# Kernel optimization log

Hardware: AMD Instinct MI355X
Metric: run time of the kernel (lower is better)

## Reference

```python
import jax, jax.numpy as jnp
import numpy as np

B, S, D, H = 8, 1024, 512, 8  # batch, max_mol_real, d_model, num_heads
DH = D // 2                   # per-branch width
DEPTH = D // H                # per-head depth (64)
HH = H // 2                   # heads per branch (4)


def setup_inputs() -> dict:
    key = jax.random.key(0)
    ks = jax.random.split(key, 16)
    sc = 0.02
    inp = {
        'x': jax.random.normal(ks[0], (B, S, D), jnp.float32),
        'mask': jnp.zeros((B, 1, 1, S), jnp.float32),
        'adj': jax.random.uniform(ks[1], (B, S, S), jnp.float32),
        'dist': jax.random.uniform(ks[2], (B, S, S), jnp.float32),
        # dist branch projections (Dense(d_model/2))
        'Wq_dist': jax.random.normal(ks[3], (D, DH), jnp.float32) * sc,
        'bq_dist': jnp.zeros((DH,), jnp.float32),
        'Wk_dist': jax.random.normal(ks[4], (D, DH), jnp.float32) * sc,
        'bk_dist': jnp.zeros((DH,), jnp.float32),
        'Wv_dist': jax.random.normal(ks[5], (D, DH), jnp.float32) * sc,
        'bv_dist': jnp.zeros((DH,), jnp.float32),
        # adj branch projections
        'Wq_adj': jax.random.normal(ks[6], (D, DH), jnp.float32) * sc,
        'bq_adj': jnp.zeros((DH,), jnp.float32),
        'Wk_adj': jax.random.normal(ks[7], (D, DH), jnp.float32) * sc,
        'bk_adj': jnp.zeros((DH,), jnp.float32),
        'Wv_adj': jax.random.normal(ks[8], (D, DH), jnp.float32) * sc,
        'bv_adj': jnp.zeros((DH,), jnp.float32),
        # output projection Dense(d_model)
        'Wo': jax.random.normal(ks[9], (D, D), jnp.float32) * sc,
        'bo': jnp.zeros((D,), jnp.float32),
    }
    return inp


def _split_heads(t):
    # (B, S, HH*DEPTH) -> (B, HH, S, DEPTH)
    return t.reshape(B, S, HH, DEPTH).transpose(0, 2, 1, 3)


def _sdpa_ad(q, k, v, mask, adj=None, dist=None):
    # mask: (B,1,1,S) -> additive -1e9 * mask, per original code
    m = mask * -1000000000.0
    logits = jnp.einsum('bhqd,bhkd->bhqk', q, k) / jnp.sqrt(jnp.float32(DEPTH))
    w = jax.nn.softmax(logits + m, axis=-1)  # (B, HH, S, S)
    if adj is not None:
        w = w * adj[:, None, :, :]
    if dist is not None:  # dist_value == 'original'
        w = w * jax.nn.softmax(dist[:, None, :, :] + m, axis=-1)
    return jnp.einsum('bhqk,bhkd->bhqd', w, v)


def reference(x, mask, adj, dist,
              Wq_dist, bq_dist, Wk_dist, bk_dist, Wv_dist, bv_dist,
              Wq_adj, bq_adj, Wk_adj, bk_adj, Wv_adj, bv_adj,
              Wo, bo):
    # ----- dist branch -----
    qd = _split_heads(x @ Wq_dist + bq_dist)
    kd = _split_heads(x @ Wk_dist + bk_dist)
    vd = _split_heads(x @ Wv_dist + bv_dist)
    od = _sdpa_ad(qd, kd, vd, mask, adj=None, dist=dist)
    od = od.transpose(0, 2, 1, 3).reshape(B, S, DH)
    # ----- adj branch -----
    qa = _split_heads(x @ Wq_adj + bq_adj)
    ka = _split_heads(x @ Wk_adj + bk_adj)
    va = _split_heads(x @ Wv_adj + bv_adj)
    oa = _sdpa_ad(qa, ka, va, mask, adj=adj, dist=None)
    oa = oa.transpose(0, 2, 1, 3).reshape(B, S, DH)
    # ----- concat + output dense -----
    cat = jnp.concatenate([od, oa], axis=-1)  # (B, S, D)
    return cat @ Wo + bo
```

## Files before the change

### kernel.cpp

```cpp
#include <hip/hip_runtime.h>

typedef __attribute__((ext_vector_type(8))) short bf16x8;
typedef __attribute__((ext_vector_type(4))) float f32x4;
typedef unsigned short ushortT;

#define B_   8
#define S_   1024
#define D_   512
#define DH_  256
#define NH_  4
#define DEP_ 64
#define LOG2E 1.4426950408889634f

__device__ __forceinline__ unsigned short f2bf(float f){
    unsigned u = __builtin_bit_cast(unsigned, f);
    u += 0x7fffu + ((u>>16)&1u);
    return (unsigned short)(u>>16);
}
__device__ __forceinline__ float bf2f(ushortT v){
    unsigned u = ((unsigned)v)<<16;
    return __builtin_bit_cast(float, u);
}
__device__ __forceinline__ int swz(int row,int cb){ return (row<<7) + (cb ^ ((row&7)<<4)); }

__global__ __launch_bounds__(256) void prep_x(const float* __restrict__ x, ushortT* __restrict__ xb){
    size_t t = (size_t)blockIdx.x*256 + threadIdx.x;
    float4 v = *(const float4*)(x + t*4);
    ushort4 o; o.x=f2bf(v.x); o.y=f2bf(v.y); o.z=f2bf(v.z); o.w=f2bf(v.w);
    *(ushort4*)(xb + t*4) = o;
}

__global__ __launch_bounds__(256) void prep_w(
    const float* __restrict__ W0, const float* __restrict__ W1, const float* __restrict__ W2,
    const float* __restrict__ W3, const float* __restrict__ W4, const float* __restrict__ W5,
    const float* __restrict__ B0, const float* __restrict__ B1, const float* __restrict__ B2,
    const float* __restrict__ B3, const float* __restrict__ B4, const float* __restrict__ B5,
    ushortT* __restrict__ Wt, float* __restrict__ bias_all)
{
    int t = blockIdx.x*256 + threadIdx.x;
    int k = t / 384;
    int n4 = (t - k*384)*4;
#pragma unroll
    for (int j=0;j<4;++j){
        int n = n4+j; int mat = n>>8, nc = n&255;
        const float* Wp = (mat==0)?W0:(mat==1)?W1:(mat==2)?W2:(mat==3)?W3:(mat==4)?W4:W5;
        Wt[(size_t)n*512 + k] = f2bf(Wp[(size_t)k*256 + nc]);
    }
    if (t < 384){
#pragma unroll
        for (int j=0;j<4;++j){
            int n = n4+j; int mat = n>>8, nc = n&255;
            const float* Bp = (mat==0)?B0:(mat==1)?B1:(mat==2)?B2:(mat==3)?B3:(mat==4)?B4:B5;
            bias_all[n] = Bp[nc];
        }
    }
}

__global__ __launch_bounds__(256) void prep_wo(const float* __restrict__ Wo, ushortT* __restrict__ Wot){
    __shared__ float t[32][33];
    const int k0 = blockIdx.y*32, n0 = blockIdx.x*32;
    const int ty = threadIdx.x>>5, tx = threadIdx.x&31;
#pragma unroll
    for (int i=0;i<4;++i)
        t[ty+8*i][tx] = Wo[(size_t)(k0+ty+8*i)*512 + n0+tx];
    __syncthreads();
#pragma unroll
    for (int i=0;i<4;++i)
        Wot[(size_t)(n0+ty+8*i)*512 + k0+tx] = f2bf(t[tx][ty+8*i]);
}

__global__ __launch_bounds__(256) void dist_sm(
    const float* __restrict__ dist, const float* __restrict__ mask, ushortT* __restrict__ Md)
{
    __shared__ ushortT pl[4][1024];
    const int bx = blockIdx.x;
    const int g  = bx&3, w = (bx>>2)&3, qb = (bx>>4)&15, b = bx>>8;
    const int r  = threadIdx.x>>6, lane = threadIdx.x&63;
    const int q  = qb*64 + 16*w + 4*g + r;
    const float* drow = dist + ((size_t)(b*1024 + q))*S_;
    const float* mrow = mask + (size_t)b*S_;

    float v[16];
    float mx = -1e30f;
#pragma unroll
    for (int j=0;j<4;++j){
        const int idx = j*256 + lane*4;
        float4 d = *(const float4*)(drow + idx);
        float4 mk = *(const float4*)(mrow + idx);
        v[j*4+0] = fmaf(mk.x, -1e9f, d.x); v[j*4+1] = fmaf(mk.y, -1e9f, d.y);
        v[j*4+2] = fmaf(mk.z, -1e9f, d.z); v[j*4+3] = fmaf(mk.w, -1e9f, d.w);
#pragma unroll
        for (int i=0;i<4;++i) mx = fmaxf(mx, v[j*4+i]);
    }
    mx = fmaxf(mx, __shfl_xor(mx,1));  mx = fmaxf(mx, __shfl_xor(mx,2));
    mx = fmaxf(mx, __shfl_xor(mx,4));  mx = fmaxf(mx, __shfl_xor(mx,8));
    mx = fmaxf(mx, __shfl_xor(mx,16)); mx = fmaxf(mx, __shfl_xor(mx,32));
    float s = 0.f;
#pragma unroll
    for (int i=0;i<16;++i){ v[i] = __builtin_exp2f((v[i]-mx)*LOG2E); s += v[i]; }
    s += __shfl_xor(s,1);  s += __shfl_xor(s,2);  s += __shfl_xor(s,4);
    s += __shfl_xor(s,8);  s += __shfl_xor(s,16); s += __shfl_xor(s,32);
    const float rcp = 1.f/s;
#pragma unroll
    for (int j=0;j<4;++j){
        ushort4 o;
        o.x=f2bf(v[j*4+0]*rcp); o.y=f2bf(v[j*4+1]*rcp);
        o.z=f2bf(v[j*4+2]*rcp); o.w=f2bf(v[j*4+3]*rcp);
        *(ushort4*)(&pl[r][(j*256 + lane*4) ^ (r<<2)]) = o;
    }
    __syncthreads();

    const int t = threadIdx.x;
    const int e = t>>4, j = t&15, kt = j>>2, r2 = j&3;
    ushortT* obase = Md + ((size_t)((b*16+qb)*16)*4 + w)*1024 + g*256 + t;
#pragma unroll
    for (int s2=0;s2<16;++s2)
        obase[(size_t)s2*4096] = pl[r2][(64*s2 + 16*kt + e) ^ (r2<<2)];
}

__global__ __launch_bounds__(256) void shuf_adj(
    const float* __restrict__ adj, ushortT* __restrict__ Ma)
{
    __shared__ ushortT tl[64][72];
    const int bx = blockIdx.x;
    const int s = bx&15, qb = (bx>>4)&15, b = bx>>8;
    const int t = threadIdx.x;
    {
        const int qr = t>>2, c0 = (t&3)*16;
        const float* src = adj + ((size_t)(b*1024 + qb*64 + qr))*S_ + 64*s + c0;
#pragma unroll
        for (int i=0;i<4;++i){
            float4 d = *(const float4*)(src + 4*i);
            tl[qr][c0+4*i+0]=f2bf(d.x); tl[qr][c0+4*i+1]=f2bf(d.y);
            tl[qr][c0+4*i+2]=f2bf(d.z); tl[qr][c0+4*i+3]=f2bf(d.w);
        }
    }
    __syncthreads();
    const int w2 = t>>6, l = t&63, g = l>>4, e = l&15;
    ushortT o[16];
#pragma unroll
    for (int j=0;j<16;++j)
        o[j] = tl[16*w2 + 4*g + (j&3)][16*(j>>2) + e];
    ushortT* dst = Ma + ((size_t)bx*4 + w2)*1024 + l*16;
    *(uint4*)(dst)     = *(uint4*)(&o[0]);
    *(uint4*)(dst + 8) = *(uint4*)(&o[8]);
}

__global__ __launch_bounds__(256) void qkv_mfma(
    const ushortT* __restrict__ xb, const ushortT* __restrict__ Wt,
    const float* __restrict__ bias_all,
    ushortT* __restrict__ q_d, ushortT* __restrict__ k_d, ushortT* __restrict__ vt_d,
    ushortT* __restrict__ q_a, ushortT* __restrict__ k_a, ushortT* __restrict__ vt_a)
{
    __shared__ __align__(16) char sm[32768];
    const int tid = threadIdx.x;
    const int w = tid>>6, l = tid&63, g = l>>4, e = l&15;
    const int wm = w>>1, wn = w&1;
    const int n0 = blockIdx.x*128, m0 = blockIdx.y*128;

    f32x4 acc[4][4];
#pragma unroll
    for (int i=0;i<4;++i)
#pragma unroll
        for (int j=0;j<4;++j) acc[i][j] = (f32x4){0.f,0.f,0.f,0.f};

    for (int k0=0;k0<512;k0+=64){
        __syncthreads();
#pragma unroll
        for (int i=0;i<4;++i){
            int fi = tid + i*256;
            int row = fi>>3, f = fi&7;
            *(uint4*)(sm + swz(row, f*16))         = *(const uint4*)(xb + ((size_t)(m0+row)*512 + k0 + 8*f));
            *(uint4*)(sm + 16384 + swz(row, f*16)) = *(const uint4*)(Wt + ((size_t)(n0+row)*512 + k0 + 8*f));
        }
        __syncthreads();
#pragma unroll
        for (int c=0;c<2;++c){
            bf16x8 a[4];
#pragma unroll
            for (int mt=0;mt<4;++mt)
                a[mt] = *(const bf16x8*)(sm + swz(64*wm + 16*mt + e, g*16 + 64*c));
#pragma unroll
            for (int nt=0;nt<4;++nt){
                bf16x8 bfr = *(const bf16x8*)(sm + 16384 + swz(64*wn + 16*nt + e, g*16 + 64*c));
#pragma unroll
                for (int mt=0;mt<4;++mt)
                    acc[mt][nt] = __builtin_amdgcn_mfma_f32_16x16x32_bf16(a[mt], bfr, acc[mt][nt], 0,0,0);
            }
        }
    }

#pragma unroll
    for (int nt=0;nt<4;++nt){
        int n = n0 + 64*wn + 16*nt + e;
        int mat = n>>8, nc = n&255, h = nc>>6, d = nc&63;
        float bi = bias_all[n];
        ushortT* base = (mat==0)?q_d:(mat==1)?k_d:(mat==2)?vt_d:(mat==3)?q_a:(mat==4)?k_a:vt_a;
        bool isV = (mat==2)||(mat==5);
#pragma unroll
        for (int mt=0;mt<4;++mt){
#pragma unroll
            for (int r=0;r<4;++r){
                int m = m0 + 64*wm + 16*mt + 4*g + r;
                int b = m>>10, s = m&1023;
                unsigned short val = f2bf(acc[mt][nt][r] + bi);
                size_t off = isV ? ((size_t)((b*NH_+h)*DEP_ + d)*S_ + s)
                                 : ((size_t)((b*NH_+h)*S_ + s)*DEP_ + d);
                base[off] = val;
            }
        }
    }
}

__global__ __launch_bounds__(256,4) void attn_mfma(
    const ushortT* __restrict__ q_d, const ushortT* __restrict__ k_d, const ushortT* __restrict__ vt_d,
    const ushortT* __restrict__ q_a, const ushortT* __restrict__ k_a, const ushortT* __restrict__ vt_a,
    const ushortT* __restrict__ Md, const ushortT* __restrict__ Ma,
    const float* __restrict__ mask, ushortT* __restrict__ cat)
{
    __shared__ __align__(16) char sm[28672];
    float* Msk = (float*)(sm + 24576);

    const int tid = threadIdx.x;
    const int w = tid>>6, l = tid&63, g = l>>4, e = l&15;
    const int bz = blockIdx.y;
    const int br = bz>>5;
    const int bh = bz&31, b = bh>>2, h = bh&3;
    const int qb = blockIdx.x;
    const int q0 = qb*64;

    const ushortT* Qg = br ? q_a  : q_d;
    const ushortT* Kg = br ? k_a  : k_d;
    const ushortT* Vg = br ? vt_a : vt_d;

    const ushortT* Qb = Qg + ((size_t)bh*S_ + q0)*DEP_;
    const ushortT* Kb = Kg + (size_t)bh*S_*DEP_;
    const ushortT* Vb = Vg + (size_t)bh*DEP_*S_;
    const ushortT* Mbase = (br ? Ma : Md) + ((size_t)((b*16+qb)*16)*4 + w)*1024 + l*16;
    const float*   mkb = mask + (size_t)b*S_;

    const int srow = tid>>3, sf = tid&7;
    const int srow2 = srow+32;

    bf16x8 aq0 = *(const bf16x8*)(Qb + (size_t)(16*w+e)*DEP_ + 8*g);
    bf16x8 aq1 = *(const bf16x8*)(Qb + (size_t)(16*w+e)*DEP_ + 8*g + 32);

    for (int i=tid;i<S_;i+=256) Msk[i] = mkb[i] * (-1e9f*LOG2E);

    uint4 kreg0 = *(const uint4*)(Kb + (size_t)srow*DEP_ + 8*sf);
    uint4 kreg1 = *(const uint4*)(Kb + (size_t)srow2*DEP_ + 8*sf);
    uint4 vreg0 = *(const uint4*)(Vb + (size_t)srow*S_  + 8*sf);
    uint4 vreg1 = *(const uint4*)(Vb + (size_t)srow2*S_ + 8*sf);
    bf16x8 mc0 = *(const bf16x8*)(Mbase);
    bf16x8 mc1 = *(const bf16x8*)(Mbase + 8);

    float z1[4];
#pragma unroll
    for (int r=0;r<4;++r) z1[r]=0.f;
    f32x4 oacc[4];
#pragma unroll
    for (int dt=0;dt<4;++dt) oacc[dt] = (f32x4){0.f,0.f,0.f,0.f};

    for (int s=0;s<16;++s){
        const int k0 = s*64;
        __syncthreads();
        *(uint4*)(sm +        swz(srow,  sf*16)) = kreg0;
        *(uint4*)(sm +        swz(srow2, sf*16)) = kreg1;
        *(uint4*)(sm + 8192 + swz(srow,  sf*16)) = vreg0;
        *(uint4*)(sm + 8192 + swz(srow2, sf*16)) = vreg1;
        __syncthreads();

        const int kn = (s<15) ? k0+64 : 0;
        kreg0 = *(const uint4*)(Kb + (size_t)(kn+srow)*DEP_ + 8*sf);
        kreg1 = *(const uint4*)(Kb + (size_t)(kn+srow2)*DEP_ + 8*sf);
        vreg0 = *(const uint4*)(Vb + (size_t)srow*S_  + kn + 8*sf);
        vreg1 = *(const uint4*)(Vb + (size_t)srow2*S_ + kn + 8*sf);
        const size_t mo = (size_t)((s<15)?s+1:0)*4096;
        bf16x8 mn0 = *(const bf16x8*)(Mbase + mo);
        bf16x8 mn1 = *(const bf16x8*)(Mbase + mo + 8);

        f32x4 lg[4];
#pragma unroll
        for (int kt=0;kt<4;++kt) lg[kt] = (f32x4){0.f,0.f,0.f,0.f};
        __builtin_amdgcn_s_setprio(1);
#pragma unroll
        for (int kt=0;kt<4;++kt){
            bf16x8 bk0 = *(const bf16x8*)(sm + swz(16*kt + e, g*16));
            bf16x8 bk1 = *(const bf16x8*)(sm + swz(16*kt + e, g*16 + 64));
            lg[kt] = __builtin_amdgcn_mfma_f32_16x16x32_bf16(aq0, bk0, lg[kt], 0,0,0);
            lg[kt] = __builtin_amdgcn_mfma_f32_16x16x32_bf16(aq1, bk1, lg[kt], 0,0,0);
        }
        __builtin_amdgcn_s_setprio(0);

        float msk2[4];
#pragma unroll
        for (int kt=0;kt<4;++kt) msk2[kt] = Msk[k0 + 16*kt + e];

#pragma unroll
        for (int r=0;r<4;++r){
            float e1[4];
#pragma unroll
            for (int kt=0;kt<4;++kt)
                e1[kt] = __builtin_exp2f(fmaf(lg[kt][r], 0.125f*LOG2E, msk2[kt]));
            z1[r] += (e1[0]+e1[1]) + (e1[2]+e1[3]);
#pragma unroll
            for (int kt=0;kt<4;++kt){
                const int j = kt*4+r;
                const float mj = bf2f((ushortT)(j<8 ? mc0[j] : mc1[j-8]));
                *(ushortT*)(sm + 16384 + 2048*w + swz(4*g + r, (16*kt+e)*2)) = f2bf(e1[kt]*mj);
            }
        }
        mc0 = mn0; mc1 = mn1;

        __builtin_amdgcn_s_setprio(1);
#pragma unroll
        for (int c=0;c<2;++c){
            bf16x8 ap = *(const bf16x8*)(sm + 16384 + 2048*w + swz(e, g*16 + 64*c));
#pragma unroll
            for (int dt=0;dt<4;++dt){
                bf16x8 bv = *(const bf16x8*)(sm + 8192 + swz(16*dt + e, g*16 + 64*c));
                oacc[dt] = __builtin_amdgcn_mfma_f32_16x16x32_bf16(ap, bv, oacc[dt], 0,0,0);
            }
        }
        __builtin_amdgcn_s_setprio(0);
    }

#pragma unroll
    for (int r=0;r<4;++r){
        z1[r] += __shfl_xor(z1[r],1); z1[r] += __shfl_xor(z1[r],2);
        z1[r] += __shfl_xor(z1[r],4); z1[r] += __shfl_xor(z1[r],8);
    }
    float inv[4];
#pragma unroll
    for (int r=0;r<4;++r) inv[r] = 1.f/z1[r];
    const int coff = br*DH_;
#pragma unroll
    for (int dt=0;dt<4;++dt){
#pragma unroll
        for (int r=0;r<4;++r){
            int q = q0 + 16*w + 4*g + r;
            int c = coff + h*DEP_ + 16*dt + e;
            cat[((size_t)b*S_ + q)*D_ + c] = f2bf(oacc[dt][r]*inv[r]);
        }
    }
}

__global__ __launch_bounds__(256) void out_mfma(
    const ushortT* __restrict__ catb, const ushortT* __restrict__ Wot,
    const float* __restrict__ bo, float* __restrict__ out)
{
    __shared__ __align__(16) char sm[32768];
    const int tid = threadIdx.x;
    const int w = tid>>6, l = tid&63, g = l>>4, e = l&15;
    const int wm = w>>1, wn = w&1;
    const int n0 = blockIdx.x*128, m0 = blockIdx.y*128;

    f32x4 acc[4][4];
#pragma unroll
    for (int i=0;i<4;++i)
#pragma unroll
        for (int j=0;j<4;++j) acc[i][j] = (f32x4){0.f,0.f,0.f,0.f};

    for (int k0=0;k0<512;k0+=64){
        __syncthreads();
#pragma unroll
        for (int i=0;i<4;++i){
            int fi = tid + i*256;
            int row = fi>>3, f = fi&7;
            *(uint4*)(sm + swz(row, f*16))         = *(const uint4*)(catb + ((size_t)(m0+row)*512 + k0 + 8*f));
            *(uint4*)(sm + 16384 + swz(row, f*16)) = *(const uint4*)(Wot  + ((size_t)(n0+row)*512 + k0 + 8*f));
        }
        __syncthreads();
#pragma unroll
        for (int c=0;c<2;++c){
            bf16x8 a[4];
#pragma unroll
            for (int mt=0;mt<4;++mt)
                a[mt] = *(const bf16x8*)(sm + swz(64*wm + 16*mt + e, g*16 + 64*c));
#pragma unroll
            for (int nt=0;nt<4;++nt){
                bf16x8 bfr = *(const bf16x8*)(sm + 16384 + swz(64*wn + 16*nt + e, g*16 + 64*c));
#pragma unroll
                for (int mt=0;mt<4;++mt)
                    acc[mt][nt] = __builtin_amdgcn_mfma_f32_16x16x32_bf16(a[mt], bfr, acc[mt][nt], 0,0,0);
            }
        }
    }

#pragma unroll
    for (int nt=0;nt<4;++nt){
        int n = n0 + 64*wn + 16*nt + e;
        float bi = bo[n];
#pragma unroll
        for (int mt=0;mt<4;++mt){
#pragma unroll
            for (int r=0;r<4;++r){
                int m = m0 + 64*wm + 16*mt + 4*g + r;
                out[(size_t)m*512 + n] = acc[mt][nt][r] + bi;
            }
        }
    }
}

extern "C" void kernel_launch(void* const* d_in, const int* in_sizes, int n_in,
                              void* d_out, int out_size, void* d_ws, size_t ws_size,
                              hipStream_t stream)
{
    (void)in_sizes; (void)n_in; (void)out_size; (void)ws_size;

    const float* x    = (const float*)d_in[0];
    const float* mask = (const float*)d_in[1];
    const float* adj  = (const float*)d_in[2];
    const float* dist = (const float*)d_in[3];
    const float* Wqd  = (const float*)d_in[4];  const float* bqd = (const float*)d_in[5];
    const float* Wkd  = (const float*)d_in[6];  const float* bkd = (const float*)d_in[7];
    const float* Wvd  = (const float*)d_in[8];  const float* bvd = (const float*)d_in[9];
    const float* Wqa  = (const float*)d_in[10]; const float* bqa = (const float*)d_in[11];
    const float* Wka  = (const float*)d_in[12]; const float* bka = (const float*)d_in[13];
    const float* Wva  = (const float*)d_in[14]; const float* bva = (const float*)d_in[15];
    const float* Wo   = (const float*)d_in[16]; const float* bo  = (const float*)d_in[17];
    float* out = (float*)d_out;

    char* W = (char*)d_ws;
    ushortT* xb   = (ushortT*)(W + 0);
    ushortT* catb = (ushortT*)(W + 0);
    ushortT* Wt   = (ushortT*)(W + 8388608);
    ushortT* Ma   = (ushortT*)(W + 8388608);
    ushortT* Wot  = (ushortT*)(W + 8388608);
    float*   bias = (float*)  (W + 9961472);
    ushortT* q_d  = (ushortT*)(W + 25165824);
    ushortT* k_d  = (ushortT*)(W + 29360128);
    ushortT* vt_d = (ushortT*)(W + 33554432);
    ushortT* q_a  = (ushortT*)(W + 37748736);
    ushortT* k_a  = (ushortT*)(W + 41943040);
    ushortT* vt_a = (ushortT*)(W + 46137344);
    ushortT* Md   = (ushortT*)(W + 50331648);

    prep_x<<<4096, 256, 0, stream>>>(x, xb);
    prep_w<<<768, 256, 0, stream>>>(Wqd,Wkd,Wvd,Wqa,Wka,Wva,
                                    bqd,bkd,bvd,bqa,bka,bva, Wt, bias);
    dist_sm<<<2048, 256, 0, stream>>>(dist, mask, Md);
    qkv_mfma<<<dim3(12,64), 256, 0, stream>>>(xb, Wt, bias, q_d,k_d,vt_d, q_a,k_a,vt_a);
    shuf_adj<<<2048, 256, 0, stream>>>(adj, Ma);
    attn_mfma<<<dim3(16,64), 256, 0, stream>>>(q_d,k_d,vt_d, q_a,k_a,vt_a,
                                               Md, Ma, mask, catb);
    prep_wo<<<dim3(16,16), 256, 0, stream>>>(Wo, Wot);
    out_mfma<<<dim3(4,64), 256, 0, stream>>>(catb, Wot, bo, out);
}
```

Baseline: 139.9 us.

## Transpose QK MFMA output so softmax probabilities pack into wide LDS stores

Swaps the A/B operands of the QK^T MFMA so each lane holds four consecutive key columns for one query row. This lets the probability tile be packed with perm into 32-bit LDS writes instead of scattered 16-bit stores, and lets the mask be read as float4. The row-sum reduction changes to a per-lane accumulator followed by cross-group shuffles. The dist softmax and adj shuffle kernels are reworked to emit the matching multiplier layout with vectorised ushort4 reads and writes, and dist_sm now processes 16 rows per block in a grid a quarter the size. The layout change spans the precompute kernels and the attention kernel, so any mismatch between them would give wrong results.

```diff
diff --git a/kernel.cpp b/kernel.cpp
--- a/kernel.cpp
+++ b/kernel.cpp
@@ -21,6 +21,7 @@
     unsigned u = ((unsigned)v)<<16;
     return __builtin_bit_cast(float, u);
 }
+__device__ __forceinline__ unsigned fbits(float f){ return __builtin_bit_cast(unsigned, f); }
 __device__ __forceinline__ int swz(int row,int cb){ return (row<<7) + (cb ^ ((row&7)<<4)); }
 
 __global__ __launch_bounds__(256) void prep_x(const float* __restrict__ x, ushortT* __restrict__ xb){
@@ -72,50 +73,55 @@
 __global__ __launch_bounds__(256) void dist_sm(
     const float* __restrict__ dist, const float* __restrict__ mask, ushortT* __restrict__ Md)
 {
-    __shared__ ushortT pl[4][1024];
+    __shared__ ushortT pl[16][1032];
     const int bx = blockIdx.x;
-    const int g  = bx&3, w = (bx>>2)&3, qb = (bx>>4)&15, b = bx>>8;
-    const int r  = threadIdx.x>>6, lane = threadIdx.x&63;
-    const int q  = qb*64 + 16*w + 4*g + r;
-    const float* drow = dist + ((size_t)(b*1024 + q))*S_;
+    const int w = bx&3, qb = (bx>>2)&15, b = bx>>6;
+    const int wd = threadIdx.x>>6, lane = threadIdx.x&63;
     const float* mrow = mask + (size_t)b*S_;
 
-    float v[16];
-    float mx = -1e30f;
-#pragma unroll
-    for (int j=0;j<4;++j){
-        const int idx = j*256 + lane*4;
-        float4 d = *(const float4*)(drow + idx);
-        float4 mk = *(const float4*)(mrow + idx);
-        v[j*4+0] = fmaf(mk.x, -1e9f, d.x); v[j*4+1] = fmaf(mk.y, -1e9f, d.y);
-        v[j*4+2] = fmaf(mk.z, -1e9f, d.z); v[j*4+3] = fmaf(mk.w, -1e9f, d.w);
-#pragma unroll
-        for (int i=0;i<4;++i) mx = fmaxf(mx, v[j*4+i]);
-    }
-    mx = fmaxf(mx, __shfl_xor(mx,1));  mx = fmaxf(mx, __shfl_xor(mx,2));
-    mx = fmaxf(mx, __shfl_xor(mx,4));  mx = fmaxf(mx, __shfl_xor(mx,8));
-    mx = fmaxf(mx, __shfl_xor(mx,16)); mx = fmaxf(mx, __shfl_xor(mx,32));
-    float s = 0.f;
-#pragma unroll
-    for (int i=0;i<16;++i){ v[i] = __builtin_exp2f((v[i]-mx)*LOG2E); s += v[i]; }
-    s += __shfl_xor(s,1);  s += __shfl_xor(s,2);  s += __shfl_xor(s,4);
-    s += __shfl_xor(s,8);  s += __shfl_xor(s,16); s += __shfl_xor(s,32);
-    const float rcp = 1.f/s;
-#pragma unroll
-    for (int j=0;j<4;++j){
-        ushort4 o;
-        o.x=f2bf(v[j*4+0]*rcp); o.y=f2bf(v[j*4+1]*rcp);
-        o.z=f2bf(v[j*4+2]*rcp); o.w=f2bf(v[j*4+3]*rcp);
-        *(ushort4*)(&pl[r][(j*256 + lane*4) ^ (r<<2)]) = o;
+    for (int rr=0; rr<4; ++rr){
+        const int er = 4*wd + rr;
+        const int q = qb*64 + 16*w + er;
+        const float* drow = dist + ((size_t)(b*1024 + q))*S_;
+        float v[16];
+        float mx = -1e30f;
+#pragma unroll
+        for (int j=0;j<4;++j){
+            const int idx = j*256 + lane*4;
+            float4 d = *(const float4*)(drow + idx);
+            float4 mk = *(const float4*)(mrow + idx);
+            v[j*4+0] = fmaf(mk.x, -1e9f, d.x); v[j*4+1] = fmaf(mk.y, -1e9f, d.y);
+            v[j*4+2] = fmaf(mk.z, -1e9f, d.z); v[j*4+3] = fmaf(mk.w, -1e9f, d.w);
+#pragma unroll
+            for (int i=0;i<4;++i) mx = fmaxf(mx, v[j*4+i]);
+        }
+        mx = fmaxf(mx, __shfl_xor(mx,1));  mx = fmaxf(mx, __shfl_xor(mx,2));
+        mx = fmaxf(mx, __shfl_xor(mx,4));  mx = fmaxf(mx, __shfl_xor(mx,8));
+        mx = fmaxf(mx, __shfl_xor(mx,16)); mx = fmaxf(mx, __shfl_xor(mx,32));
+        float s = 0.f;
+#pragma unroll
+        for (int i=0;i<16;++i){ v[i] = __builtin_exp2f((v[i]-mx)*LOG2E); s += v[i]; }
+        s += __shfl_xor(s,1);  s += __shfl_xor(s,2);  s += __shfl_xor(s,4);
+        s += __shfl_xor(s,8);  s += __shfl_xor(s,16); s += __shfl_xor(s,32);
+        const float rcp = 1.f/s;
+#pragma unroll
+        for (int j=0;j<4;++j){
+            ushort4 o;
+            o.x=f2bf(v[j*4+0]*rcp); o.y=f2bf(v[j*4+1]*rcp);
+            o.z=f2bf(v[j*4+2]*rcp); o.w=f2bf(v[j*4+3]*rcp);
+            *(ushort4*)(&pl[er][j*256 + lane*4]) = o;
+        }
     }
     __syncthreads();
 
     const int t = threadIdx.x;
-    const int e = t>>4, j = t&15, kt = j>>2, r2 = j&3;
-    ushortT* obase = Md + ((size_t)((b*16+qb)*16)*4 + w)*1024 + g*256 + t;
-#pragma unroll
-    for (int s2=0;s2<16;++s2)
-        obase[(size_t)s2*4096] = pl[r2][(64*s2 + 16*kt + e) ^ (r2<<2)];
+    const int e2 = (t>>2)&15, kt2 = t&3, g2 = t>>6;
+    ushortT* slab = Md + (((size_t)(b*16+qb)*16)*4 + w)*1024;
+#pragma unroll
+    for (int s2=0;s2<16;++s2){
+        ushort4 vv = *(const ushort4*)(&pl[e2][64*s2 + 16*kt2 + 4*g2]);
+        *(ushort4*)(slab + (size_t)s2*4096 + t*4) = vv;
+    }
 }
 
 __global__ __launch_bounds__(256) void shuf_adj(
@@ -139,9 +145,9 @@
     const int w2 = t>>6, l = t&63, g = l>>4, e = l&15;
     ushortT o[16];
 #pragma unroll
-    for (int j=0;j<16;++j)
-        o[j] = tl[16*w2 + 4*g + (j&3)][16*(j>>2) + e];
-    ushortT* dst = Ma + ((size_t)bx*4 + w2)*1024 + l*16;
+    for (int kt=0;kt<4;++kt)
+        *(ushort4*)(&o[4*kt]) = *(const ushort4*)(&tl[16*w2 + e][16*kt + 4*g]);
+    ushortT* dst = Ma + ((((size_t)(b*16+qb)*16 + s)*4 + w2)*1024) + l*16;
     *(uint4*)(dst)     = *(uint4*)(&o[0]);
     *(uint4*)(dst + 8) = *(uint4*)(&o[8]);
 }
@@ -254,9 +260,7 @@
     bf16x8 mc0 = *(const bf16x8*)(Mbase);
     bf16x8 mc1 = *(const bf16x8*)(Mbase + 8);
 
-    float z1[4];
-#pragma unroll
-    for (int r=0;r<4;++r) z1[r]=0.f;
+    float zl = 0.f;
     f32x4 oacc[4];
 #pragma unroll
     for (int dt=0;dt<4;++dt) oacc[dt] = (f32x4){0.f,0.f,0.f,0.f};
@@ -287,28 +291,33 @@
         for (int kt=0;kt<4;++kt){
             bf16x8 bk0 = *(const bf16x8*)(sm + swz(16*kt + e, g*16));
             bf16x8 bk1 = *(const bf16x8*)(sm + swz(16*kt + e, g*16 + 64));
-            lg[kt] = __builtin_amdgcn_mfma_f32_16x16x32_bf16(aq0, bk0, lg[kt], 0,0,0);
-            lg[kt] = __builtin_amdgcn_mfma_f32_16x16x32_bf16(aq1, bk1, lg[kt], 0,0,0);
+            lg[kt] = __builtin_amdgcn_mfma_f32_16x16x32_bf16(bk0, aq0, lg[kt], 0,0,0);
+            lg[kt] = __builtin_amdgcn_mfma_f32_16x16x32_bf16(bk1, aq1, lg[kt], 0,0,0);
         }
         __builtin_amdgcn_s_setprio(0);
 
-        float msk2[4];
-#pragma unroll
-        for (int kt=0;kt<4;++kt) msk2[kt] = Msk[k0 + 16*kt + e];
-
-#pragma unroll
-        for (int r=0;r<4;++r){
-            float e1[4];
-#pragma unroll
-            for (int kt=0;kt<4;++kt)
-                e1[kt] = __builtin_exp2f(fmaf(lg[kt][r], 0.125f*LOG2E, msk2[kt]));
-            z1[r] += (e1[0]+e1[1]) + (e1[2]+e1[3]);
-#pragma unroll
-            for (int kt=0;kt<4;++kt){
-                const int j = kt*4+r;
+        f32x4 mskv[4];
+#pragma unroll
+        for (int kt=0;kt<4;++kt)
+            mskv[kt] = *(const f32x4*)(Msk + k0 + 16*kt + 4*g);
+
+#pragma unroll
+        for (int kt=0;kt<4;++kt){
+            float e1[4], pm[4];
+#pragma unroll
+            for (int r=0;r<4;++r)
+                e1[r] = __builtin_exp2f(fmaf(lg[kt][r], 0.125f*LOG2E, mskv[kt][r]));
+            zl += (e1[0]+e1[1]) + (e1[2]+e1[3]);
+#pragma unroll
+            for (int r=0;r<4;++r){
+                const int j = 4*kt + r;
                 const float mj = bf2f((ushortT)(j<8 ? mc0[j] : mc1[j-8]));
-                *(ushortT*)(sm + 16384 + 2048*w + swz(4*g + r, (16*kt+e)*2)) = f2bf(e1[kt]*mj);
-            }
+                pm[r] = e1[r]*mj;
+            }
+            unsigned w0 = __builtin_amdgcn_perm(fbits(pm[1]), fbits(pm[0]), 0x07060302u);
+            unsigned w1 = __builtin_amdgcn_perm(fbits(pm[3]), fbits(pm[2]), 0x07060302u);
+            *(unsigned*)(sm + 16384 + 2048*w + swz(e, 32*kt + 8*g))     = w0;
+            *(unsigned*)(sm + 16384 + 2048*w + swz(e, 32*kt + 8*g + 4)) = w1;
         }
         mc0 = mn0; mc1 = mn1;
 
@@ -325,14 +334,12 @@
         __builtin_amdgcn_s_setprio(0);
     }
 
-#pragma unroll
-    for (int r=0;r<4;++r){
-        z1[r] += __shfl_xor(z1[r],1); z1[r] += __shfl_xor(z1[r],2);
-        z1[r] += __shfl_xor(z1[r],4); z1[r] += __shfl_xor(z1[r],8);
-    }
+    zl += __shfl_xor(zl,16); zl += __shfl_xor(zl,32);
     float inv[4];
 #pragma unroll
-    for (int r=0;r<4;++r) inv[r] = 1.f/z1[r];
+    for (int r=0;r<4;++r)
+        inv[r] = 1.f / __shfl(zl, (l & 48) | (4*g + r));
+
     const int coff = br*DH_;
 #pragma unroll
     for (int dt=0;dt<4;++dt){
@@ -439,7 +446,7 @@
     prep_x<<<4096, 256, 0, stream>>>(x, xb);
     prep_w<<<768, 256, 0, stream>>>(Wqd,Wkd,Wvd,Wqa,Wka,Wva,
                                     bqd,bkd,bvd,bqa,bka,bva, Wt, bias);
-    dist_sm<<<2048, 256, 0, stream>>>(dist, mask, Md);
+    dist_sm<<<512, 256, 0, stream>>>(dist, mask, Md);
     qkv_mfma<<<dim3(12,64), 256, 0, stream>>>(xb, Wt, bias, q_d,k_d,vt_d, q_a,k_a,vt_a);
     shuf_adj<<<2048, 256, 0, stream>>>(adj, Ma);
     attn_mfma<<<dim3(16,64), 256, 0, stream>>>(q_d,k_d,vt_d, q_a,k_a,vt_a,
```

After: 137.5 us. Within noise of the previous version (-1.8%).
